# Optimization experiments

Measured on AMD Instinct MI355X. Metric: run time of the kernel, lower is better.

Reference implementation:

```python
import jax, jax.numpy as jnp
import numpy as np

# Standard NF4 codebook (QLoRA), sorted ascending, values in [-1, 1]
_NF4_CODE = np.array([
    -1.0, -0.6961928009986877, -0.5250730514526367, -0.39491748809814453,
    -0.28444138169288635, -0.18477343022823334, -0.09105003625154495, 0.0,
    0.07958029955625534, 0.16093020141124725, 0.24611230194568634,
    0.33791524171829224, 0.44070982933044434, 0.5626170039176941,
    0.7229568362236023, 1.0], dtype=np.float32)

BLOCK = 64           # NF4 block size (per-block absmax scale)
SCALE_BLOCK = 256    # double-quant: scales quantized to 8 bits per 256 scales


def nf4_quant_dequant(w):
    """Fake NF4 quantize->dequantize of weight [out, in] (QLoRA, block=64,
    8-bit double-quantized scales per 256 blocks)."""
    out_dim, in_dim = w.shape
    code = jnp.asarray(_NF4_CODE, dtype=w.dtype)
    wb = w.reshape(-1, BLOCK)                              # [nb, 64]
    absmax = jnp.max(jnp.abs(wb), axis=1)                  # [nb]
    # double quantization of scales: 8-bit symmetric per scale block
    sb = absmax.reshape(-1, SCALE_BLOCK)                   # [nsb, 256]
    s_amax = jnp.max(sb, axis=1, keepdims=True)
    s_amax = jnp.where(s_amax == 0, 1.0, s_amax)
    q8 = jnp.clip(jnp.round(sb / s_amax * 127.0), -127, 127)
    scale_dq = (q8 / 127.0 * s_amax).reshape(-1, 1)        # [nb, 1]
    # quantize normalized weights to nearest NF4 code (midpoint search)
    safe_absmax = jnp.where(absmax == 0, 1.0, absmax)[:, None]
    norm = wb / safe_absmax                                # in [-1, 1]
    boundaries = (code[:-1] + code[1:]) * 0.5              # [15]
    idx = jnp.searchsorted(boundaries, norm)               # nearest code index
    w_dq = code[idx] * scale_dq                            # dequantize
    return w_dq.reshape(out_dim, in_dim)


def setup_inputs() -> dict:
    key = jax.random.key(0)
    kx, kw = jax.random.split(key)
    x = jax.random.normal(kx, (16384, 4096), dtype=jnp.float32)
    weight = jax.random.normal(kw, (4096, 4096), dtype=jnp.float32) * 0.02
    return {"x": x, "weight": weight}


def reference(x, weight):
    # forward: F.linear(x, dequantize(nf4_quantize(weight)))
    w_dq = nf4_quant_dequant(weight)
    return x @ w_dq.T  # [tokens, out_dim]
```

## Files before the change

kernel.cpp:

```cpp
#include <hip/hip_runtime.h>
#include <stdint.h>


typedef __bf16 bf16x8 __attribute__((ext_vector_type(8)));
typedef float f32x4 __attribute__((ext_vector_type(4)));

constexpr float NF4_CODE[16] = {
    -1.0f, -0.6961928009986877f, -0.5250730514526367f, -0.39491748809814453f,
    -0.28444138169288635f, -0.18477343022823334f, -0.09105003625154495f, 0.0f,
    0.07958029955625534f, 0.16093020141124725f, 0.24611230194568634f,
    0.33791524171829224f, 0.44070982933044434f, 0.5626170039176941f,
    0.7229568362236023f, 1.0f};
constexpr float NF4_BND[15] = {
    0.5f * (NF4_CODE[0] + NF4_CODE[1]),   0.5f * (NF4_CODE[1] + NF4_CODE[2]),
    0.5f * (NF4_CODE[2] + NF4_CODE[3]),   0.5f * (NF4_CODE[3] + NF4_CODE[4]),
    0.5f * (NF4_CODE[4] + NF4_CODE[5]),   0.5f * (NF4_CODE[5] + NF4_CODE[6]),
    0.5f * (NF4_CODE[6] + NF4_CODE[7]),   0.5f * (NF4_CODE[7] + NF4_CODE[8]),
    0.5f * (NF4_CODE[8] + NF4_CODE[9]),   0.5f * (NF4_CODE[9] + NF4_CODE[10]),
    0.5f * (NF4_CODE[10] + NF4_CODE[11]), 0.5f * (NF4_CODE[11] + NF4_CODE[12]),
    0.5f * (NF4_CODE[12] + NF4_CODE[13]), 0.5f * (NF4_CODE[13] + NF4_CODE[14]),
    0.5f * (NF4_CODE[14] + NF4_CODE[15])};

__device__ __forceinline__ unsigned short f2bf(float f) {
  unsigned int u = __float_as_uint(f);
  u += 0x7fffu + ((u >> 16) & 1u);
  return (unsigned short)(u >> 16);
}

__global__ __launch_bounds__(256) void nf4_dequant(const float* __restrict__ w,
                                                   unsigned short* __restrict__ wdq) {
  __shared__ float s_am[256];
  __shared__ float s_red[4];
  __shared__ float s_code[16];
  const int t = threadIdx.x;
  if (t < 16) s_code[t] = NF4_CODE[t];
  const size_t base = (size_t)blockIdx.x * 16384;
  const f32x4* src = (const f32x4*)(w + base);

  f32x4 v[16];
#pragma unroll
  for (int k = 0; k < 16; ++k) {
    v[k] = __builtin_nontemporal_load(src + k * 256 + t);
    float m = fmaxf(fmaxf(fabsf(v[k][0]), fabsf(v[k][1])),
                    fmaxf(fabsf(v[k][2]), fabsf(v[k][3])));
    m = fmaxf(m, __shfl_xor(m, 1));
    m = fmaxf(m, __shfl_xor(m, 2));
    m = fmaxf(m, __shfl_xor(m, 4));
    m = fmaxf(m, __shfl_xor(m, 8));
    if ((t & 15) == 0) s_am[k * 16 + (t >> 4)] = m;
  }
  __syncthreads();
  float m = s_am[t];
  m = fmaxf(m, __shfl_xor(m, 1));
  m = fmaxf(m, __shfl_xor(m, 2));
  m = fmaxf(m, __shfl_xor(m, 4));
  m = fmaxf(m, __shfl_xor(m, 8));
  m = fmaxf(m, __shfl_xor(m, 16));
  m = fmaxf(m, __shfl_xor(m, 32));
  if ((t & 63) == 0) s_red[t >> 6] = m;
  __syncthreads();
  const float s_amax = fmaxf(fmaxf(s_red[0], s_red[1]), fmaxf(s_red[2], s_red[3]));
  const float sa = (s_amax == 0.f) ? 1.f : s_amax;

#pragma unroll
  for (int k = 0; k < 16; ++k) {
    const float am = s_am[k * 16 + (t >> 4)];
    float q8 = rintf(am / sa * 127.f);
    q8 = fminf(fmaxf(q8, -127.f), 127.f);
    const float scale = (q8 / 127.f) * sa;
    const float safe_am = (am == 0.f) ? 1.f : am;
    unsigned r[4];
#pragma unroll
    for (int e = 0; e < 4; ++e) {
      const float norm = v[k][e] / safe_am;
      int idx = 0;
#pragma unroll
      for (int j = 0; j < 15; ++j) idx += (NF4_BND[j] < norm) ? 1 : 0;
      r[e] = (unsigned)f2bf(s_code[idx] * scale);
    }
    uint2 o;
    o.x = r[0] | (r[1] << 16);
    o.y = r[2] | (r[3] << 16);
    ((uint2*)(wdq + base))[k * 256 + t] = o;
  }
}

__global__ __launch_bounds__(256) void cast_f32_to_bf16(const float* __restrict__ x,
                                                        unsigned short* __restrict__ y,
                                                        size_t n8) {
  const size_t stride = (size_t)gridDim.x * 256;
  for (size_t i = (size_t)blockIdx.x * 256 + threadIdx.x; i < n8; i += stride) {
    const f32x4* s = (const f32x4*)x + i * 2;
    const f32x4 a = __builtin_nontemporal_load(s);
    const f32x4 b = __builtin_nontemporal_load(s + 1);
    uint4 o;
    o.x = (unsigned)f2bf(a[0]) | ((unsigned)f2bf(a[1]) << 16);
    o.y = (unsigned)f2bf(a[2]) | ((unsigned)f2bf(a[3]) << 16);
    o.z = (unsigned)f2bf(b[0]) | ((unsigned)f2bf(b[1]) << 16);
    o.w = (unsigned)f2bf(b[2]) | ((unsigned)f2bf(b[3]) << 16);
    ((uint4*)y)[i] = o;
  }
}


__device__ __forceinline__ void gld16(const unsigned short* g, unsigned short* l) {
  __builtin_amdgcn_global_load_lds(
      (__attribute__((address_space(1))) void*)g,
      (__attribute__((address_space(3))) void*)l, 16, 0, 0);
}

#define BARX                                                                   \
  do {                                                                         \
    asm volatile("" ::: "memory");                                             \
    __builtin_amdgcn_s_barrier();                                              \
    asm volatile("" ::: "memory");                                             \
  } while (0)
#define VMW(n) asm volatile("s_waitcnt vmcnt(" #n ")" ::: "memory")
#define SP1 __builtin_amdgcn_s_setprio(1)
#define SP0 __builtin_amdgcn_s_setprio(0)

#define STG(buf, ab, hf, ks)                                                   \
  do {                                                                         \
    const unsigned short* g_ =                                                 \
        ((ab) ? gB0 : gA0) + (size_t)(hf)*HOFF + (size_t)(ks);                 \
    unsigned short* l_ =                                                       \
        lds + (buf)*32768 + (ab)*16384 + (hf)*8192 + wvoff;                    \
    gld16(g_, l_);                                                             \
    gld16(g_ + 64 * (size_t)K, l_ + 4096);                                     \
  } while (0)

#define RDA(buf, mh, ks)                                                       \
  do {                                                                         \
    _Pragma("unroll") for (int i4 = 0; i4 < 4; ++i4) {                         \
      afr[i4][ks] = *(const bf16x8*)(pa + (buf)*32768 + (mh)*4096 +            \
                                     i4 * 1024 + ((ks) ? aoff1 : aoff0));      \
    }                                                                          \
  } while (0)

#define RDB(buf, nh, ks)                                                       \
  do {                                                                         \
    _Pragma("unroll") for (int j2 = 0; j2 < 2; ++j2) {                         \
      bfr[(nh)*2 + j2][ks] = *(const bf16x8*)(pb + (buf)*32768 + (nh)*2048 +   \
                                              j2 * 1024 +                      \
                                              ((ks) ? aoff1 : aoff0));         \
    }                                                                          \
  } while (0)

#define MMH(mh, nh, ks)                                                        \
  do {                                                                         \
    _Pragma("unroll") for (int i4 = 0; i4 < 4; ++i4) {                         \
      _Pragma("unroll") for (int j2 = 0; j2 < 2; ++j2) {                       \
        acc[(mh)*4 + i4][(nh)*2 + j2] =                                        \
            __builtin_amdgcn_mfma_f32_16x16x32_bf16(                           \
                afr[i4][ks], bfr[(nh)*2 + j2][ks],                             \
                acc[(mh)*4 + i4][(nh)*2 + j2], 0, 0, 0);                       \
      }                                                                        \
    }                                                                          \
  } while (0)

__global__ __launch_bounds__(512, 2) void gemm8p(const unsigned short* __restrict__ A,
                                                 const unsigned short* __restrict__ Bt,
                                                 float* __restrict__ C,
                                                 int M, int N, int K) {
  __shared__ __align__(16) unsigned short lds[65536];

  const int t = threadIdx.x;
  const int wave = t >> 6;
  const int lane = t & 63;

  const int nbx = N >> 8;
  const int nwg = nbx * (M >> 8);
  const int q8 = nwg >> 3, r8 = nwg & 7;
  const int xcd = (int)blockIdx.x & 7, off = (int)blockIdx.x >> 3;
  const int wg =
      (xcd < r8 ? xcd * (q8 + 1) : r8 * (q8 + 1) + (xcd - r8) * q8) + off;
  const int bm = (wg / nbx) << 8;
  const int bn = (wg % nbx) << 8;

  const size_t HOFF = (size_t)128 * K;
  const int srow = wave * 8 + (lane >> 3);
  const int sj = (lane & 7) ^ (lane >> 3);
  const unsigned short* gA0 = A + (size_t)(bm + srow) * K + sj * 8;
  const unsigned short* gB0 = Bt + (size_t)(bn + srow) * K + sj * 8;
  const int wvoff = wave * 512;

  const int wm = wave >> 2;
  const int wn = wave & 3;
  const int quad = lane >> 4;
  const int lrow = lane & 15;
  const int s0 = quad ^ (lrow & 7);
  const int aoff0 = lrow * 64 + s0 * 8;
  const int aoff1 = lrow * 64 + (s0 ^ 4) * 8;
  const unsigned short* pa = lds + wm * 8192;
  const unsigned short* pb = lds + 16384 + (wn >> 1) * 8192 + (wn & 1) * 4096;

  f32x4 acc[8][4];
  const f32x4 zero = {0.f, 0.f, 0.f, 0.f};
#pragma unroll
  for (int i = 0; i < 8; ++i)
#pragma unroll
    for (int j = 0; j < 4; ++j) acc[i][j] = zero;

  bf16x8 afr[4][2];
  bf16x8 bfr[4][2];

  STG(0, 1, 0, 0); STG(0, 1, 1, 0);
  STG(0, 0, 0, 0); STG(0, 0, 1, 0);
  STG(1, 1, 0, 64); STG(1, 1, 1, 64);
  STG(1, 0, 0, 64); STG(1, 0, 1, 64);
  VMW(8);
  BARX;
  RDA(0, 0, 0); RDA(0, 0, 1);
  RDB(0, 0, 0); RDB(0, 0, 1);

  const int niter = K >> 7;
  for (int it = 0; it < niter; ++it) {
    const int kt = it << 7;
    int kc2 = kt + 128; if (kc2 > K - 64) kc2 = K - 64;
    int kc3 = kt + 192; if (kc3 > K - 64) kc3 = K - 64;

    VMW(8); BARX;
    SP1; MMH(0, 0, 0); RDB(0, 1, 0); MMH(0, 0, 1); RDB(0, 1, 1); SP0;
    VMW(8); STG(0, 1, 0, kc2); STG(0, 1, 1, kc2); BARX;
    SP1; MMH(0, 1, 0); RDA(0, 1, 0); MMH(0, 1, 1); RDA(0, 1, 1); SP0;
    VMW(8); STG(0, 0, 0, kc2); STG(0, 0, 1, kc2); BARX;
    SP1; MMH(1, 0, 0); RDB(1, 0, 0); MMH(1, 0, 1); RDB(1, 0, 1); SP0;
    VMW(8); BARX;
    SP1; MMH(1, 1, 0); RDA(1, 0, 0); MMH(1, 1, 1); RDA(1, 0, 1); SP0;
    VMW(8); BARX;
    SP1; MMH(0, 0, 0); RDB(1, 1, 0); MMH(0, 0, 1); RDB(1, 1, 1); SP0;
    VMW(8); STG(1, 1, 0, kc3); STG(1, 1, 1, kc3); BARX;
    SP1; MMH(0, 1, 0); RDA(1, 1, 0); MMH(0, 1, 1); RDA(1, 1, 1); SP0;
    VMW(8); STG(1, 0, 0, kc3); STG(1, 0, 1, kc3); BARX;
    SP1; MMH(1, 0, 0); RDB(0, 0, 0); MMH(1, 0, 1); RDB(0, 0, 1); SP0;
    VMW(8); BARX;
    SP1; MMH(1, 1, 0); RDA(0, 0, 0); MMH(1, 1, 1); RDA(0, 0, 1); SP0;
  }

  VMW(0);

  const int crow = bm + wm * 128 + quad * 4;
  const int ccol = bn + wn * 64 + lrow;
#pragma unroll
  for (int i = 0; i < 8; ++i) {
#pragma unroll
    for (int j = 0; j < 4; ++j) {
      float* cp = C + (size_t)(crow + i * 16) * N + (ccol + j * 16);
#pragma unroll
      for (int r = 0; r < 4; ++r)
        __builtin_nontemporal_store(acc[i][j][r], cp + (size_t)r * N);
    }
  }
}

extern "C" void kernel_launch(void* const* d_in, const int* in_sizes, int n_in,
                              void* d_out, int out_size, void* d_ws, size_t ws_size,
                              hipStream_t stream) {
  const float* x = (const float*)d_in[0];
  const float* w = (const float*)d_in[1];
  const int K = 4096;
  const int M = in_sizes[0] / K;
  const int N = in_sizes[1] / K;

  unsigned short* wdq = (unsigned short*)d_ws;
  unsigned short* xbf = wdq + (size_t)in_sizes[1];

  nf4_dequant<<<in_sizes[1] / 16384, 256, 0, stream>>>(w, wdq);
  cast_f32_to_bf16<<<4096, 256, 0, stream>>>(x, xbf, (size_t)in_sizes[0] / 8);
  dim3 grid((N / 256) * (M / 256));
  gemm8p<<<grid, 512, 0, stream>>>(xbf, wdq, (float*)d_out, M, N, K);
}
```

Measured before the change: 863.8 us.

## Fuse fp32-to-bf16 activation cast into GEMM A-tile loading

```diff
diff --git a/kernel.cpp b/kernel.cpp
--- a/kernel.cpp
+++ b/kernel.cpp
@@ -27,8 +27,8 @@
   return (unsigned short)(u >> 16);
 }
 
-__global__ __launch_bounds__(256) void nf4_dequant(const float* __restrict__ w,
-                                                   unsigned short* __restrict__ wdq) {
+__global__ __launch_bounds__(256) void prep(const float* __restrict__ w,
+                                            unsigned short* __restrict__ wdq) {
   __shared__ float s_am[256];
   __shared__ float s_red[4];
   __shared__ float s_code[16];
@@ -59,7 +59,8 @@
   m = fmaxf(m, __shfl_xor(m, 32));
   if ((t & 63) == 0) s_red[t >> 6] = m;
   __syncthreads();
-  const float s_amax = fmaxf(fmaxf(s_red[0], s_red[1]), fmaxf(s_red[2], s_red[3]));
+  const float s_amax =
+      fmaxf(fmaxf(s_red[0], s_red[1]), fmaxf(s_red[2], s_red[3]));
   const float sa = (s_amax == 0.f) ? 1.f : s_amax;
 
 #pragma unroll
@@ -85,23 +86,6 @@
   }
 }
 
-__global__ __launch_bounds__(256) void cast_f32_to_bf16(const float* __restrict__ x,
-                                                        unsigned short* __restrict__ y,
-                                                        size_t n8) {
-  const size_t stride = (size_t)gridDim.x * 256;
-  for (size_t i = (size_t)blockIdx.x * 256 + threadIdx.x; i < n8; i += stride) {
-    const f32x4* s = (const f32x4*)x + i * 2;
-    const f32x4 a = __builtin_nontemporal_load(s);
-    const f32x4 b = __builtin_nontemporal_load(s + 1);
-    uint4 o;
-    o.x = (unsigned)f2bf(a[0]) | ((unsigned)f2bf(a[1]) << 16);
-    o.y = (unsigned)f2bf(a[2]) | ((unsigned)f2bf(a[3]) << 16);
-    o.z = (unsigned)f2bf(b[0]) | ((unsigned)f2bf(b[1]) << 16);
-    o.w = (unsigned)f2bf(b[2]) | ((unsigned)f2bf(b[3]) << 16);
-    ((uint4*)y)[i] = o;
-  }
-}
-
 
 __device__ __forceinline__ void gld16(const unsigned short* g, unsigned short* l) {
   __builtin_amdgcn_global_load_lds(
@@ -116,17 +100,36 @@
     asm volatile("" ::: "memory");                                             \
   } while (0)
 #define VMW(n) asm volatile("s_waitcnt vmcnt(" #n ")" ::: "memory")
+#define LGKM0 asm volatile("s_waitcnt lgkmcnt(0)" ::: "memory")
+#define SCHB __builtin_amdgcn_sched_barrier(0)
 #define SP1 __builtin_amdgcn_s_setprio(1)
 #define SP0 __builtin_amdgcn_s_setprio(0)
 
-#define STG(buf, ab, hf, ks)                                                   \
-  do {                                                                         \
-    const unsigned short* g_ =                                                 \
-        ((ab) ? gB0 : gA0) + (size_t)(hf)*HOFF + (size_t)(ks);                 \
-    unsigned short* l_ =                                                       \
-        lds + (buf)*32768 + (ab)*16384 + (hf)*8192 + wvoff;                    \
+#define STGB(buf, hf, ks)                                                      \
+  do {                                                                         \
+    const unsigned short* g_ = gB0 + (size_t)(hf)*HOFF + (size_t)(ks);         \
+    unsigned short* l_ = lds + (buf)*32768 + 16384 + (hf)*8192 + wvoff;        \
     gld16(g_, l_);                                                             \
     gld16(g_ + 64 * (size_t)K, l_ + 4096);                                     \
+  } while (0)
+
+#define LDA(ks)                                                                \
+  do {                                                                         \
+    const f32x4* g_ = (const f32x4*)(gAx + (size_t)(ks));                      \
+    _Pragma("unroll") for (int q = 0; q < 8; ++q) rA[q] = g_[q];               \
+  } while (0)
+
+#define CVTW(buf)                                                              \
+  do {                                                                         \
+    _Pragma("unroll") for (int c = 0; c < 4; ++c) {                            \
+      bf16x8 wv;                                                               \
+      _Pragma("unroll") for (int e = 0; e < 4; ++e) {                          \
+        wv[e] = (__bf16)rA[c * 2][e];                                          \
+        wv[e + 4] = (__bf16)rA[c * 2 + 1][e];                                  \
+      }                                                                        \
+      const int slot = (((lane & 1) << 2) + c) ^ r7;                           \
+      *(bf16x8*)(ldsA + (buf)*32768 + slot * 8) = wv;                          \
+    }                                                                          \
   } while (0)
 
 #define RDA(buf, mh, ks)                                                       \
@@ -158,7 +161,7 @@
     }                                                                          \
   } while (0)
 
-__global__ __launch_bounds__(512, 2) void gemm8p(const unsigned short* __restrict__ A,
+__global__ __launch_bounds__(512, 2) void gemm8p(const float* __restrict__ A,
                                                  const unsigned short* __restrict__ Bt,
                                                  float* __restrict__ C,
                                                  int M, int N, int K) {
@@ -180,9 +183,15 @@
   const size_t HOFF = (size_t)128 * K;
   const int srow = wave * 8 + (lane >> 3);
   const int sj = (lane & 7) ^ (lane >> 3);
-  const unsigned short* gA0 = A + (size_t)(bm + srow) * K + sj * 8;
   const unsigned short* gB0 = Bt + (size_t)(bn + srow) * K + sj * 8;
   const int wvoff = wave * 512;
+
+  const int arowg = wave * 32 + (lane >> 1);
+  const float* gAx = A + (size_t)(bm + arowg) * K + (lane & 1) * 32;
+  const int r7 = arowg & 7;
+  unsigned short* ldsA =
+      lds + ((arowg >> 7) * 8192) + (arowg & 127) * 64;
+  f32x4 rA[8];
 
   const int wm = wave >> 2;
   const int wn = wave & 3;
@@ -204,12 +213,15 @@
   bf16x8 afr[4][2];
   bf16x8 bfr[4][2];
 
-  STG(0, 1, 0, 0); STG(0, 1, 1, 0);
-  STG(0, 0, 0, 0); STG(0, 0, 1, 0);
-  STG(1, 1, 0, 64); STG(1, 1, 1, 64);
-  STG(1, 0, 0, 64); STG(1, 0, 1, 64);
+  LDA(0);
+  STGB(0, 0, 0); STGB(0, 1, 0);
+  STGB(1, 0, 64); STGB(1, 1, 64);
   VMW(8);
-  BARX;
+  CVTW(0);
+  LDA(64);
+  VMW(0);
+  CVTW(1);
+  LGKM0; BARX;
   RDA(0, 0, 0); RDA(0, 0, 1);
   RDB(0, 0, 0); RDB(0, 0, 1);
 
@@ -219,21 +231,21 @@
     int kc2 = kt + 128; if (kc2 > K - 64) kc2 = K - 64;
     int kc3 = kt + 192; if (kc3 > K - 64) kc3 = K - 64;
 
-    VMW(8); BARX;
+    LDA(kc2); BARX;
     SP1; MMH(0, 0, 0); RDB(0, 1, 0); MMH(0, 0, 1); RDB(0, 1, 1); SP0;
-    VMW(8); STG(0, 1, 0, kc2); STG(0, 1, 1, kc2); BARX;
+    STGB(0, 0, kc2); STGB(0, 1, kc2); BARX;
     SP1; MMH(0, 1, 0); RDA(0, 1, 0); MMH(0, 1, 1); RDA(0, 1, 1); SP0;
-    VMW(8); STG(0, 0, 0, kc2); STG(0, 0, 1, kc2); BARX;
+    VMW(4); BARX; SCHB; CVTW(0);
     SP1; MMH(1, 0, 0); RDB(1, 0, 0); MMH(1, 0, 1); RDB(1, 0, 1); SP0;
-    VMW(8); BARX;
+    LGKM0; BARX;
     SP1; MMH(1, 1, 0); RDA(1, 0, 0); MMH(1, 1, 1); RDA(1, 0, 1); SP0;
-    VMW(8); BARX;
+    LDA(kc3); BARX;
     SP1; MMH(0, 0, 0); RDB(1, 1, 0); MMH(0, 0, 1); RDB(1, 1, 1); SP0;
-    VMW(8); STG(1, 1, 0, kc3); STG(1, 1, 1, kc3); BARX;
+    STGB(1, 0, kc3); STGB(1, 1, kc3); BARX;
     SP1; MMH(0, 1, 0); RDA(1, 1, 0); MMH(0, 1, 1); RDA(1, 1, 1); SP0;
-    VMW(8); STG(1, 0, 0, kc3); STG(1, 0, 1, kc3); BARX;
+    VMW(4); BARX; SCHB; CVTW(1);
     SP1; MMH(1, 0, 0); RDB(0, 0, 0); MMH(1, 0, 1); RDB(0, 0, 1); SP0;
-    VMW(8); BARX;
+    LGKM0; BARX;
     SP1; MMH(1, 1, 0); RDA(0, 0, 0); MMH(1, 1, 1); RDA(0, 0, 1); SP0;
   }
 
@@ -263,10 +275,8 @@
   const int N = in_sizes[1] / K;
 
   unsigned short* wdq = (unsigned short*)d_ws;
-  unsigned short* xbf = wdq + (size_t)in_sizes[1];
-
-  nf4_dequant<<<in_sizes[1] / 16384, 256, 0, stream>>>(w, wdq);
-  cast_f32_to_bf16<<<4096, 256, 0, stream>>>(x, xbf, (size_t)in_sizes[0] / 8);
+
+  prep<<<in_sizes[1] / 16384, 256, 0, stream>>>(w, wdq);
   dim3 grid((N / 256) * (M / 256));
-  gemm8p<<<grid, 512, 0, stream>>>(xbf, wdq, (float*)d_out, M, N, K);
-}
+  gemm8p<<<grid, 512, 0, stream>>>(x, wdq, (float*)d_out, M, N, K);
+}
```

After: 1.373 ms. 59.0% more time.
